# Optimization experiments

Hardware: AMD Instinct MI355X
Metric: run time of the kernel (lower is better)

The kernel has to match this reference:

```python
import jax, jax.numpy as jnp
import numpy as np

B, S, E, H = 2, 2048, 1024, 16
D = E // H  # head_dim = 64


def setup_inputs() -> dict:
    key = jax.random.key(0)
    ks = jax.random.split(key, 5)
    return {
        "hidden_states": jax.random.normal(ks[0], (B, S, E), jnp.float32),
        "c_attn_w": jax.random.normal(ks[1], (E, 3 * E), jnp.float32) * 0.02,
        "c_attn_b": jnp.zeros((3 * E,), jnp.float32),
        "c_proj_w": jax.random.normal(ks[2], (E, E), jnp.float32) * 0.02,
        "c_proj_b": jnp.zeros((E,), jnp.float32),
    }


def reference(hidden_states, c_attn_w, c_attn_b, c_proj_w, c_proj_b):
    # Conv1D: x @ w + b -> qkv [B, S, 3E]
    qkv = hidden_states @ c_attn_w + c_attn_b
    q, k, v = jnp.split(qkv, 3, axis=-1)
    # [B, H, S, D]
    q = q.reshape(B, S, H, D).transpose(0, 2, 1, 3)
    k = k.reshape(B, S, H, D).transpose(0, 2, 1, 3)
    v = v.reshape(B, S, H, D).transpose(0, 2, 1, 3)
    # scores [B, H, S, S], scaled by sqrt(head_dim)
    scores = jnp.einsum("bhqd,bhkd->bhqk", q, k) / jnp.sqrt(jnp.asarray(D, q.dtype))
    causal = jnp.tril(jnp.ones((S, S), bool))  # [S, S]
    mask_value = jnp.finfo(scores.dtype).min
    scores = jnp.where(causal, scores, mask_value)
    attn = jax.nn.softmax(scores, axis=-1)
    # attn @ V -> [B, H, S, D] -> [B, S, E]
    out = jnp.einsum("bhqk,bhkd->bhqd", attn, v)
    out = out.transpose(0, 2, 1, 3).reshape(B, S, E)
    return out @ c_proj_w + c_proj_b
```

## Files before the change

### kernel.cpp

```cpp
#include <hip/hip_runtime.h>

using bf16 = __bf16;
typedef __bf16 bf16x8 __attribute__((ext_vector_type(8)));
typedef __bf16 bf16x4 __attribute__((ext_vector_type(4)));
typedef float  f32x4  __attribute__((ext_vector_type(4)));

#define MFMA16(a, b, c) __builtin_amdgcn_mfma_f32_16x16x32_bf16((a), (b), (c), 0, 0, 0)

static constexpr int S = 2048, E = 1024;
static constexpr float CSCALE = 0.18033688011112042f;

__device__ __forceinline__ void gld16(const bf16* g, bf16* l) {
    __builtin_amdgcn_global_load_lds((const __attribute__((address_space(1))) unsigned*)g,
                                     (__attribute__((address_space(3))) unsigned*)l, 16, 0, 0);
}

__global__ __launch_bounds__(256) void k_prep(const float* __restrict__ hs, const float* __restrict__ w0,
                                              const float* __restrict__ w1, bf16* __restrict__ A0,
                                              bf16* __restrict__ Wt0, bf16* __restrict__ Wt1) {
    __shared__ float tile[32][33];
    const int bx = blockIdx.x;
    if (bx < 4096) {
        int i = (bx * 256 + threadIdx.x) * 4;
        float4 v = *(const float4*)(hs + i);
        bf16x4 o = { (bf16)v.x, (bf16)v.y, (bf16)v.z, (bf16)v.w };
        *(bf16x4*)(A0 + i) = o;
        return;
    }
    const float* in;
    bf16* outp;
    int K, N, nb, kb;
    if (bx < 4096 + 3072) {
        int j = bx - 4096; in = w0; outp = Wt0; K = 1024; N = 3072; nb = j % 96; kb = j / 96;
    } else {
        int j = bx - 7168; in = w1; outp = Wt1; K = 1024; N = 1024; nb = j % 32; kb = j / 32;
    }
    const int bxx = nb * 32, byy = kb * 32;
    const int tx = threadIdx.x & 31, ty = threadIdx.x >> 5;
#pragma unroll
    for (int i = 0; i < 32; i += 8)
        tile[ty + i][tx] = in[(long)(byy + ty + i) * N + bxx + tx];
    __syncthreads();
#pragma unroll
    for (int i = 0; i < 32; i += 8)
        outp[(long)(bxx + ty + i) * K + byy + tx] = (bf16)tile[tx][ty + i];
}

__global__ __launch_bounds__(384, 3) void k_gemm_qkv(const bf16* __restrict__ A, const bf16* __restrict__ Bt,
                                                     const float* __restrict__ bias, bf16* __restrict__ Qs,
                                                     bf16* __restrict__ Kf, bf16* __restrict__ Vf, int Kk) {
    __shared__ __align__(16) char smem[61440];
    bf16* sA = (bf16*)smem;
    bf16* sB = (bf16*)(smem + 24576);

    const int NT = Kk >> 5;

    const int bid = blockIdx.x;
    const int sid = (bid & 7) * 64 + (bid >> 3);
    const long bm = (long)(sid & 31) * 128;
    const long bn = (long)(sid >> 5) * 192;

    const int tid = threadIdx.x;
    const int w = tid >> 6, lane = tid & 63;
    const int col = lane & 15, quad = lane >> 4;
    const int wc = w % 3, wr = w / 3;
    const int wrow = wr * 64, wcol = wc * 64;

    const int nch = (w < 2) ? 4 : 3;
    const bf16* gsrc[4];
    bf16* ldst[4];
    int sstep[4];
#pragma unroll
    for (int j = 0; j < 4; ++j) {
        const int c = w + 6 * j;
        const bool a = (c < 8);
        const int cl = a ? c : (c - 8);
        const int r = cl * 16 + (lane >> 2);
        const int kc = (lane & 3) ^ ((r >> 1) & 3);
        gsrc[j] = (a ? A + (bm + r) * Kk : Bt + (bn + r) * Kk) + kc * 8;
        ldst[j] = (a ? sA : sB) + r * 32 + (lane & 3) * 8;
        sstep[j] = a ? 4096 : 6144;
    }

    f32x4 acc[4][4] = {};

#pragma unroll
    for (int tt = 0; tt < 2; ++tt)
#pragma unroll
        for (int j = 0; j < 4; ++j)
            if (j < nch) gld16(gsrc[j] + tt * 32, ldst[j] + tt * sstep[j]);
    if (w < 2) asm volatile("s_waitcnt vmcnt(4)" ::: "memory");
    else       asm volatile("s_waitcnt vmcnt(3)" ::: "memory");
    __builtin_amdgcn_s_barrier();

    int slot = 0, wslot = 2;
#pragma unroll 1
    for (int t = 0; t < NT; ++t) {
        const bf16* sAs = sA + slot * 4096;
        const bf16* sBs = sB + slot * 6144;

        if (t + 2 < NT) {
#pragma unroll
            for (int j = 0; j < 4; ++j)
                if (j < nch) gld16(gsrc[j] + (t + 2) * 32, ldst[j] + wslot * sstep[j]);
        }

        bf16x8 af[4], bfr[4];
#pragma unroll
        for (int mt = 0; mt < 4; ++mt) {
            const int row = wrow + mt * 16 + col;
            af[mt] = *(const bf16x8*)(sAs + row * 32 + ((quad ^ ((row >> 1) & 3)) * 8));
        }
#pragma unroll
        for (int nt = 0; nt < 4; ++nt) {
            const int row = wcol + nt * 16 + col;
            bfr[nt] = *(const bf16x8*)(sBs + row * 32 + ((quad ^ ((row >> 1) & 3)) * 8));
        }
        __builtin_amdgcn_s_barrier();
        __builtin_amdgcn_s_setprio(1);
#pragma unroll
        for (int mt = 0; mt < 4; ++mt)
#pragma unroll
            for (int nt = 0; nt < 4; ++nt)
                acc[mt][nt] = MFMA16(af[mt], bfr[nt], acc[mt][nt]);
        __builtin_amdgcn_s_setprio(0);
        if (t < NT - 2) {
            if (w < 2) asm volatile("s_waitcnt vmcnt(4)" ::: "memory");
            else       asm volatile("s_waitcnt vmcnt(3)" ::: "memory");
        } else {
            asm volatile("s_waitcnt vmcnt(0)" ::: "memory");
        }
        __builtin_amdgcn_s_barrier();

        slot = (slot == 2) ? 0 : slot + 1;
        wslot = (wslot == 2) ? 0 : wslot + 1;
    }

    const long gc0 = bn + wcol;
    const int seg = (int)(gc0 >> 10);
    float bv[4];
#pragma unroll
    for (int nt = 0; nt < 4; ++nt) bv[nt] = bias[gc0 + nt * 16 + col];

    if (seg == 0) {
#pragma unroll
        for (int nt = 0; nt < 4; ++nt) {
            const long gc = gc0 + nt * 16 + col;
#pragma unroll
            for (int mt = 0; mt < 4; ++mt) {
                const long gr = bm + wrow + mt * 16 + quad * 4;
#pragma unroll
                for (int r = 0; r < 4; ++r)
                    Qs[(gr + r) * 1024 + gc] = (bf16)((acc[mt][nt][r] + bv[nt]) * CSCALE);
            }
        }
        return;
    }

    bf16* myT = (bf16*)smem + w * 4608;
    const int bmi = (int)bm;
    const int b = bmi >> 11;
    const int ktw = ((bmi & 2047) >> 6) + wr;
    const int head = (int)((gc0 & 1023) >> 6);
    const int bh = b * 16 + head;

    if (seg == 1) {
#pragma unroll
        for (int mt = 0; mt < 4; ++mt)
#pragma unroll
            for (int nt = 0; nt < 4; ++nt)
#pragma unroll
                for (int r = 0; r < 4; ++r)
                    myT[(mt * 16 + quad * 4 + r) * 72 + nt * 16 + col] = (bf16)(acc[mt][nt][r] + bv[nt]);
#pragma unroll
        for (int mtp = 0; mtp < 4; ++mtp)
#pragma unroll
            for (int half = 0; half < 2; ++half) {
                bf16x8 ch = *(const bf16x8*)(myT + (mtp * 16 + col) * 72 + half * 32 + quad * 8);
                const long chunk = ((long)(bh * 32 + ktw) * 8 + mtp * 2 + half) * 64 + lane;
                *(bf16x8*)(Kf + chunk * 8) = ch;
            }
    } else {
#pragma unroll
        for (int nt = 0; nt < 4; ++nt)
#pragma unroll
            for (int mt = 0; mt < 4; ++mt) {
                bf16x4 pk = { (bf16)(acc[mt][nt][0] + bv[nt]), (bf16)(acc[mt][nt][1] + bv[nt]),
                              (bf16)(acc[mt][nt][2] + bv[nt]), (bf16)(acc[mt][nt][3] + bv[nt]) };
                *(bf16x4*)(myT + (nt * 16 + col) * 72 + mt * 16 + quad * 4) = pk;
            }
#pragma unroll
        for (int dt = 0; dt < 4; ++dt)
#pragma unroll
            for (int ks = 0; ks < 2; ++ks) {
                bf16x8 ch = *(const bf16x8*)(myT + (dt * 16 + col) * 72 + ks * 32 + quad * 8);
                const long chunk = ((long)(bh * 32 + ktw) * 8 + dt * 2 + ks) * 64 + lane;
                *(bf16x8*)(Vf + chunk * 8) = ch;
            }
    }
}

__global__ __launch_bounds__(256) void k_gemm_bt64(const bf16* __restrict__ A, const bf16* __restrict__ Bt,
                                                    const float* __restrict__ bias, float* __restrict__ Cout,
                                                    int Mm, int Nn, int Kk) {
    const int bm = blockIdx.x * 64;
    const int bn = blockIdx.y * 128;
    const int tid = threadIdx.x;
    const int w = tid >> 6, lane = tid & 63;
    const int wm = (w >> 1) * 32, wn = (w & 1) * 64;
    const int col = lane & 15, quad = lane >> 4;

    __shared__ bf16 sA[64 * 64];
    __shared__ bf16 sB[128 * 64];

    const bf16* pA[2]; bf16* lA[2];
#pragma unroll
    for (int i = 0; i < 2; i++) {
        const int c = i * 256 + w * 64 + lane;
        const int r = c >> 3, sl = (c & 7) ^ (r & 7);
        pA[i] = A + (long)(bm + r) * Kk + sl * 8;
        lA[i] = sA + i * 2048 + w * 512;
    }
    const bf16* pB[4]; bf16* lB[4];
#pragma unroll
    for (int i = 0; i < 4; i++) {
        const int c = i * 256 + w * 64 + lane;
        const int r = c >> 3, sl = (c & 7) ^ (r & 7);
        pB[i] = Bt + (long)(bn + r) * Kk + sl * 8;
        lB[i] = sB + i * 2048 + w * 512;
    }

    f32x4 acc[2][4] = {};

    for (int k0 = 0; k0 < Kk; k0 += 64) {
        __syncthreads();
#pragma unroll
        for (int i = 0; i < 2; i++) gld16(pA[i] + k0, lA[i]);
#pragma unroll
        for (int i = 0; i < 4; i++) gld16(pB[i] + k0, lB[i]);
        __syncthreads();
#pragma unroll
        for (int h = 0; h < 2; h++) {
            bf16x8 af[2], bfr[4];
#pragma unroll
            for (int mt = 0; mt < 2; mt++) {
                const int row = wm + mt * 16 + col;
                af[mt] = *(const bf16x8*)(sA + row * 64 + (((h * 4 + quad) ^ (col & 7)) * 8));
            }
#pragma unroll
            for (int nt = 0; nt < 4; nt++) {
                const int row = wn + nt * 16 + col;
                bfr[nt] = *(const bf16x8*)(sB + row * 64 + (((h * 4 + quad) ^ (col & 7)) * 8));
            }
#pragma unroll
            for (int mt = 0; mt < 2; mt++)
#pragma unroll
                for (int nt = 0; nt < 4; nt++)
                    acc[mt][nt] = MFMA16(af[mt], bfr[nt], acc[mt][nt]);
        }
    }

#pragma unroll
    for (int mt = 0; mt < 2; mt++) {
        const int gr = bm + wm + mt * 16 + quad * 4;
#pragma unroll
        for (int nt = 0; nt < 4; nt++) {
            const int gc = bn + wn + nt * 16 + col;
            const float bv = bias[gc];
#pragma unroll
            for (int r = 0; r < 4; r++)
                Cout[(long)(gr + r) * Nn + gc] = acc[mt][nt][r] + bv;
        }
    }
}

__global__ __launch_bounds__(128) void k_attn(const bf16* __restrict__ Qs, const bf16* __restrict__ Kf,
                                              const bf16* __restrict__ Vf, bf16* __restrict__ out) {
    const int bh = blockIdx.x & 31;
    const int tp = blockIdx.x >> 5;
    const int b = bh >> 4, h = bh & 15;
    const int tid = threadIdx.x;
    const int w = tid >> 6, lane = tid & 63;
    const int col = lane & 15, quad = lane >> 4;

    __shared__ bf16 sP[2][32 * 72];
    __shared__ float M[2][64][36];
    bf16* pw = sP[w];

    const bf16* kfb = Kf + ((long)bh << 17) + lane * 8;
    const bf16* vfb = Vf + ((long)bh << 17) + lane * 8;

#pragma unroll 1
    for (int sel = 0; sel < 2; sel++) {
        const int t = sel ? 63 - tp : tp;
        const int q0 = t * 32;
        const int nkt = (t >> 1) + 1;
        const int kA = nkt >> 1;
        const int kbeg = w ? kA : 0;
        const int kend = w ? nkt : kA;

        bf16x8 bq[2][2];
#pragma unroll
        for (int qg = 0; qg < 2; qg++) {
            const bf16* qp = Qs + (long)(b * S + q0 + qg * 16 + col) * E + h * 64 + quad * 8;
            bq[qg][0] = *(const bf16x8*)(qp);
            bq[qg][1] = *(const bf16x8*)(qp + 32);
        }
        float m_[2] = { -1e30f, -1e30f }, l_[2] = { 0.f, 0.f };
        f32x4 o[2][4] = {};

#pragma unroll 1
        for (int kt = kbeg; kt < kend; kt++) {
            bf16x8 kfr[4][2], vfr[4][2];
#pragma unroll
            for (int mt = 0; mt < 4; mt++)
#pragma unroll
                for (int half = 0; half < 2; half++)
                    kfr[mt][half] = *(const bf16x8*)(kfb + ((long)(kt * 8 + mt * 2 + half) << 9));
#pragma unroll
            for (int dt = 0; dt < 4; dt++)
#pragma unroll
                for (int ks = 0; ks < 2; ks++)
                    vfr[dt][ks] = *(const bf16x8*)(vfb + ((long)(kt * 8 + dt * 2 + ks) << 9));

            f32x4 s[2][4];
#pragma unroll
            for (int mt = 0; mt < 4; mt++)
#pragma unroll
                for (int qg = 0; qg < 2; qg++) {
                    f32x4 z = {};
                    z = MFMA16(kfr[mt][0], bq[qg][0], z);
                    z = MFMA16(kfr[mt][1], bq[qg][1], z);
                    s[qg][mt] = z;
                }
            if (kt == nkt - 1) {
#pragma unroll
                for (int qg = 0; qg < 2; qg++) {
                    const int qrow = q0 + qg * 16 + col;
#pragma unroll
                    for (int mt = 0; mt < 4; mt++)
#pragma unroll
                        for (int r = 0; r < 4; r++)
                            if (kt * 64 + mt * 16 + quad * 4 + r > qrow) s[qg][mt][r] = -1e30f;
                }
            }
#pragma unroll
            for (int qg = 0; qg < 2; qg++) {
                float cm = -1e30f;
#pragma unroll
                for (int mt = 0; mt < 4; mt++)
#pragma unroll
                    for (int r = 0; r < 4; r++) cm = fmaxf(cm, s[qg][mt][r]);
                cm = fmaxf(cm, __shfl_xor(cm, 16));
                cm = fmaxf(cm, __shfl_xor(cm, 32));
                const float mnew = fmaxf(m_[qg], cm);
                const float alpha = __builtin_amdgcn_exp2f(m_[qg] - mnew);
                m_[qg] = mnew;
                float rs = 0.f;
#pragma unroll
                for (int mt = 0; mt < 4; mt++)
#pragma unroll
                    for (int r = 0; r < 4; r++) {
                        float pe = __builtin_amdgcn_exp2f(s[qg][mt][r] - mnew);
                        s[qg][mt][r] = pe;
                        rs += pe;
                    }
                l_[qg] = l_[qg] * alpha + rs;
#pragma unroll
                for (int dt = 0; dt < 4; dt++)
#pragma unroll
                    for (int r = 0; r < 4; r++) o[qg][dt][r] *= alpha;
#pragma unroll
                for (int mt = 0; mt < 4; mt++) {
                    bf16x4 pk = { (bf16)s[qg][mt][0], (bf16)s[qg][mt][1],
                                  (bf16)s[qg][mt][2], (bf16)s[qg][mt][3] };
                    *(bf16x4*)(pw + (qg * 16 + col) * 72 + mt * 16 + quad * 4) = pk;
                }
            }
#pragma unroll
            for (int ks = 0; ks < 2; ks++) {
                bf16x8 ap[2];
#pragma unroll
                for (int qg = 0; qg < 2; qg++)
                    ap[qg] = *(const bf16x8*)(pw + (qg * 16 + col) * 72 + ks * 32 + quad * 8);
#pragma unroll
                for (int dt = 0; dt < 4; dt++)
#pragma unroll
                    for (int qg = 0; qg < 2; qg++)
                        o[qg][dt] = MFMA16(vfr[dt][ks], ap[qg], o[qg][dt]);
            }
        }

#pragma unroll
        for (int qg = 0; qg < 2; qg++) {
            float lt = l_[qg];
            lt += __shfl_xor(lt, 16);
            lt += __shfl_xor(lt, 32);
            l_[qg] = lt;
        }

        if (w == 0) {
#pragma unroll
            for (int qg = 0; qg < 2; qg++) {
#pragma unroll
                for (int dt = 0; dt < 4; dt++)
                    *(f32x4*)&M[sel][lane][qg * 16 + dt * 4] = o[qg][dt];
                M[sel][lane][32 + qg * 2] = m_[qg];
                M[sel][lane][33 + qg * 2] = l_[qg];
            }
        }
        __syncthreads();
        if (w == 1) {
#pragma unroll
            for (int qg = 0; qg < 2; qg++) {
                const float m0 = M[sel][lane][32 + qg * 2];
                const float l0 = M[sel][lane][33 + qg * 2];
                const float mm = fmaxf(m0, m_[qg]);
                const float a0 = __builtin_amdgcn_exp2f(m0 - mm);
                const float a1 = __builtin_amdgcn_exp2f(m_[qg] - mm);
                const float li = 1.f / (l0 * a0 + l_[qg] * a1);
                bf16* op = out + (long)(b * S + q0 + qg * 16 + col) * E + h * 64 + quad * 4;
#pragma unroll
                for (int dt = 0; dt < 4; dt++) {
                    f32x4 o0 = *(const f32x4*)&M[sel][lane][qg * 16 + dt * 4];
                    bf16x4 ov;
#pragma unroll
                    for (int r = 0; r < 4; r++)
                        ov[r] = (bf16)((o0[r] * a0 + o[qg][dt][r] * a1) * li);
                    *(bf16x4*)(op + dt * 16) = ov;
                }
            }
        }
    }
}

extern "C" void kernel_launch(void* const* d_in, const int* in_sizes, int n_in,
                              void* d_out, int out_size, void* d_ws, size_t ws_size,
                              hipStream_t stream) {
    const float* hs = (const float*)d_in[0];
    const float* w0 = (const float*)d_in[1];
    const float* b0 = (const float*)d_in[2];
    const float* w1 = (const float*)d_in[3];
    const float* b1 = (const float*)d_in[4];
    float* outp = (float*)d_out;

    char* ws = (char*)d_ws;
    bf16* A0    = (bf16*)(ws);
    bf16* Wt0   = (bf16*)(ws + 8388608);
    bf16* Wt1   = (bf16*)(ws + 14680064);
    bf16* Qs    = (bf16*)(ws + 16777216);
    bf16* Kf    = (bf16*)(ws + 25165824);
    bf16* Vf    = (bf16*)(ws + 33554432);
    bf16* attnO = (bf16*)(ws + 41943040);

    k_prep<<<8192, 256, 0, stream>>>(hs, w0, w1, A0, Wt0, Wt1);
    k_gemm_qkv<<<512, 384, 0, stream>>>(A0, Wt0, b0, Qs, Kf, Vf, 1024);
    k_attn<<<1024, 128, 0, stream>>>(Qs, Kf, Vf, attnO);
    k_gemm_bt64<<<dim3(64, 8), 256, 0, stream>>>(attnO, Wt1, b1, outp, 4096, 1024, 1024);
}
```

Baseline: 179.0 us.

## Pre-swizzle QKV weights into MFMA fragment layout and load B directly to registers

The prep kernel now writes the QKV weight transpose in an MFMA-fragment-ordered layout. The QKV GEMM then loads each wave's B operand straight from global memory into registers with dwordx4 loads, double-buffered across two register sets, instead of staging it through LDS. LDS usage drops to the A tiles only, and the epilogue transposes in two halves to fit the smaller buffer. This removes LDS traffic and bandwidth for B and may raise occupancy. The cost is more VGPR pressure, and each wave reads its weights from global memory with no sharing across the waves that use the same columns.

```diff
diff --git a/kernel.cpp b/kernel.cpp
--- a/kernel.cpp
+++ b/kernel.cpp
@@ -13,6 +13,15 @@
 __device__ __forceinline__ void gld16(const bf16* g, bf16* l) {
     __builtin_amdgcn_global_load_lds((const __attribute__((address_space(1))) unsigned*)g,
                                      (__attribute__((address_space(3))) unsigned*)l, 16, 0, 0);
+}
+
+__device__ __forceinline__ void gload4(const bf16* p, bf16x8& r0, bf16x8& r1, bf16x8& r2, bf16x8& r3) {
+    asm volatile("global_load_dwordx4 %0, %4, off\n\t"
+                 "global_load_dwordx4 %1, %4, off offset:1024\n\t"
+                 "global_load_dwordx4 %2, %4, off offset:2048\n\t"
+                 "global_load_dwordx4 %3, %4, off offset:3072"
+                 : "=&v"(r0), "=&v"(r1), "=&v"(r2), "=&v"(r3)
+                 : "v"(p));
 }
 
 __global__ __launch_bounds__(256) void k_prep(const float* __restrict__ hs, const float* __restrict__ w0,
@@ -30,10 +39,11 @@
     const float* in;
     bf16* outp;
     int K, N, nb, kb;
+    bool frag;
     if (bx < 4096 + 3072) {
-        int j = bx - 4096; in = w0; outp = Wt0; K = 1024; N = 3072; nb = j % 96; kb = j / 96;
+        int j = bx - 4096; in = w0; outp = Wt0; K = 1024; N = 3072; nb = j % 96; kb = j / 96; frag = true;
     } else {
-        int j = bx - 7168; in = w1; outp = Wt1; K = 1024; N = 1024; nb = j % 32; kb = j / 32;
+        int j = bx - 7168; in = w1; outp = Wt1; K = 1024; N = 1024; nb = j % 32; kb = j / 32; frag = false;
     }
     const int bxx = nb * 32, byy = kb * 32;
     const int tx = threadIdx.x & 31, ty = threadIdx.x >> 5;
@@ -41,17 +51,30 @@
     for (int i = 0; i < 32; i += 8)
         tile[ty + i][tx] = in[(long)(byy + ty + i) * N + bxx + tx];
     __syncthreads();
-#pragma unroll
-    for (int i = 0; i < 32; i += 8)
-        outp[(long)(bxx + ty + i) * K + byy + tx] = (bf16)tile[tx][ty + i];
+    if (frag) {
+        if (threadIdx.x < 128) {
+            const int nl = threadIdx.x >> 2;
+            const int kq = threadIdx.x & 3;
+            const int n = bxx + nl, k = byy + kq * 8;
+            bf16x8 v;
+#pragma unroll
+            for (int e = 0; e < 8; ++e) v[e] = (bf16)tile[kq * 8 + e][nl];
+            const long addr = (((long)(n >> 6) * 32 + (k >> 5)) * 4 + ((n >> 4) & 3)) * 512
+                            + ((k >> 3) & 3) * 128 + (n & 15) * 8;
+            *(bf16x8*)(outp + addr) = v;
+        }
+    } else {
+#pragma unroll
+        for (int i = 0; i < 32; i += 8)
+            outp[(long)(bxx + ty + i) * K + byy + tx] = (bf16)tile[tx][ty + i];
+    }
 }
 
 __global__ __launch_bounds__(384, 3) void k_gemm_qkv(const bf16* __restrict__ A, const bf16* __restrict__ Bt,
                                                      const float* __restrict__ bias, bf16* __restrict__ Qs,
                                                      bf16* __restrict__ Kf, bf16* __restrict__ Vf, int Kk) {
-    __shared__ __align__(16) char smem[61440];
+    __shared__ __align__(16) char smem[28672];
     bf16* sA = (bf16*)smem;
-    bf16* sB = (bf16*)(smem + 24576);
 
     const int NT = Kk >> 5;
 
@@ -66,75 +89,70 @@
     const int wc = w % 3, wr = w / 3;
     const int wrow = wr * 64, wcol = wc * 64;
 
-    const int nch = (w < 2) ? 4 : 3;
-    const bf16* gsrc[4];
-    bf16* ldst[4];
-    int sstep[4];
-#pragma unroll
-    for (int j = 0; j < 4; ++j) {
-        const int c = w + 6 * j;
-        const bool a = (c < 8);
-        const int cl = a ? c : (c - 8);
-        const int r = cl * 16 + (lane >> 2);
-        const int kc = (lane & 3) ^ ((r >> 1) & 3);
-        gsrc[j] = (a ? A + (bm + r) * Kk : Bt + (bn + r) * Kk) + kc * 8;
-        ldst[j] = (a ? sA : sB) + r * 32 + (lane & 3) * 8;
-        sstep[j] = a ? 4096 : 6144;
-    }
+    const int u0 = w * 64 + lane;
+    const int r0s = u0 >> 2, kq0 = u0 & 3;
+    const bf16* gA0 = A + (bm + r0s) * Kk + ((kq0 ^ ((r0s >> 1) & 3)) * 8);
+    const int u1 = 384 + ((w & 1) * 64) + lane;
+    const int r1s = u1 >> 2, kq1 = u1 & 3;
+    const bf16* gA1 = A + (bm + r1s) * Kk + ((kq1 ^ ((r1s >> 1) & 3)) * 8);
+
+    const int strip = (int)(sid >> 5) * 3 + wc;
+    const bf16* wfb = Bt + (long)strip * 65536 + lane * 8;
 
     f32x4 acc[4][4] = {};
-
-#pragma unroll
-    for (int tt = 0; tt < 2; ++tt)
-#pragma unroll
-        for (int j = 0; j < 4; ++j)
-            if (j < nch) gld16(gsrc[j] + tt * 32, ldst[j] + tt * sstep[j]);
-    if (w < 2) asm volatile("s_waitcnt vmcnt(4)" ::: "memory");
-    else       asm volatile("s_waitcnt vmcnt(3)" ::: "memory");
+    bf16x8 b00, b01, b02, b03, b10, b11, b12, b13;
+
+    gld16(gA0, sA + u0 * 8);
+    if (w < 2) gld16(gA1, sA + u1 * 8);
+    gld16(gA0 + 32, sA + 4096 + u0 * 8);
+    if (w < 2) gld16(gA1 + 32, sA + 4096 + u1 * 8);
+    gload4(wfb, b00, b01, b02, b03);
+    gload4(wfb + 2048, b10, b11, b12, b13);
+    asm volatile("s_waitcnt vmcnt(4)" ::: "memory");
     __builtin_amdgcn_s_barrier();
-
-    int slot = 0, wslot = 2;
+    __builtin_amdgcn_sched_barrier(0);
+
+#define QSTEP(T, B0, B1, B2, B3) do {                                                     \
+    const int t_ = (T);                                                                   \
+    const bf16* sAs = sA + (t_ % 3) * 4096;                                               \
+    bf16x8 af0, af1, af2, af3;                                                            \
+    { const int r_ = wrow + col;      af0 = *(const bf16x8*)(sAs + r_ * 32 + ((quad ^ ((r_ >> 1) & 3)) * 8)); } \
+    { const int r_ = wrow + 16 + col; af1 = *(const bf16x8*)(sAs + r_ * 32 + ((quad ^ ((r_ >> 1) & 3)) * 8)); } \
+    { const int r_ = wrow + 32 + col; af2 = *(const bf16x8*)(sAs + r_ * 32 + ((quad ^ ((r_ >> 1) & 3)) * 8)); } \
+    { const int r_ = wrow + 48 + col; af3 = *(const bf16x8*)(sAs + r_ * 32 + ((quad ^ ((r_ >> 1) & 3)) * 8)); } \
+    const bool pf_ = (t_ + 2 < NT);                                                       \
+    if (pf_) {             \
+        bf16* dA = sA + ((t_ + 2) % 3) * 4096;                                            \
+        gld16(gA0 + (t_ + 2) * 32, dA + u0 * 8);                                          \
+        if (w < 2) gld16(gA1 + (t_ + 2) * 32, dA + u1 * 8);                               \
+    }                                                                                     \
+    __builtin_amdgcn_s_setprio(1);                                                        \
+    acc[0][0] = MFMA16(af0, B0, acc[0][0]); acc[0][1] = MFMA16(af0, B1, acc[0][1]);       \
+    acc[0][2] = MFMA16(af0, B2, acc[0][2]); acc[0][3] = MFMA16(af0, B3, acc[0][3]);       \
+    acc[1][0] = MFMA16(af1, B0, acc[1][0]); acc[1][1] = MFMA16(af1, B1, acc[1][1]);       \
+    acc[1][2] = MFMA16(af1, B2, acc[1][2]); acc[1][3] = MFMA16(af1, B3, acc[1][3]);       \
+    acc[2][0] = MFMA16(af2, B0, acc[2][0]); acc[2][1] = MFMA16(af2, B1, acc[2][1]);       \
+    acc[2][2] = MFMA16(af2, B2, acc[2][2]); acc[2][3] = MFMA16(af2, B3, acc[2][3]);       \
+    acc[3][0] = MFMA16(af3, B0, acc[3][0]); acc[3][1] = MFMA16(af3, B1, acc[3][1]);       \
+    acc[3][2] = MFMA16(af3, B2, acc[3][2]); acc[3][3] = MFMA16(af3, B3, acc[3][3]);       \
+    __builtin_amdgcn_s_setprio(0);                                                        \
+    if (pf_) gload4(wfb + (long)(t_ + 2) * 2048, B0, B1, B2, B3);   \
+    if (t_ < NT - 2) {                                                                    \
+        if (w < 2) asm volatile("s_waitcnt vmcnt(6)" ::: "memory");                       \
+        else       asm volatile("s_waitcnt vmcnt(5)" ::: "memory");                       \
+    } else {                                                                              \
+        asm volatile("s_waitcnt vmcnt(0)" ::: "memory");                                  \
+    }                                                                                     \
+    __builtin_amdgcn_s_barrier();                                                         \
+    __builtin_amdgcn_sched_barrier(0);                                                    \
+} while (0)
+
 #pragma unroll 1
-    for (int t = 0; t < NT; ++t) {
-        const bf16* sAs = sA + slot * 4096;
-        const bf16* sBs = sB + slot * 6144;
-
-        if (t + 2 < NT) {
-#pragma unroll
-            for (int j = 0; j < 4; ++j)
-                if (j < nch) gld16(gsrc[j] + (t + 2) * 32, ldst[j] + wslot * sstep[j]);
-        }
-
-        bf16x8 af[4], bfr[4];
-#pragma unroll
-        for (int mt = 0; mt < 4; ++mt) {
-            const int row = wrow + mt * 16 + col;
-            af[mt] = *(const bf16x8*)(sAs + row * 32 + ((quad ^ ((row >> 1) & 3)) * 8));
-        }
-#pragma unroll
-        for (int nt = 0; nt < 4; ++nt) {
-            const int row = wcol + nt * 16 + col;
-            bfr[nt] = *(const bf16x8*)(sBs + row * 32 + ((quad ^ ((row >> 1) & 3)) * 8));
-        }
-        __builtin_amdgcn_s_barrier();
-        __builtin_amdgcn_s_setprio(1);
-#pragma unroll
-        for (int mt = 0; mt < 4; ++mt)
-#pragma unroll
-            for (int nt = 0; nt < 4; ++nt)
-                acc[mt][nt] = MFMA16(af[mt], bfr[nt], acc[mt][nt]);
-        __builtin_amdgcn_s_setprio(0);
-        if (t < NT - 2) {
-            if (w < 2) asm volatile("s_waitcnt vmcnt(4)" ::: "memory");
-            else       asm volatile("s_waitcnt vmcnt(3)" ::: "memory");
-        } else {
-            asm volatile("s_waitcnt vmcnt(0)" ::: "memory");
-        }
-        __builtin_amdgcn_s_barrier();
-
-        slot = (slot == 2) ? 0 : slot + 1;
-        wslot = (wslot == 2) ? 0 : wslot + 1;
-    }
+    for (int t = 0; t < NT; t += 2) {
+        QSTEP(t,     b00, b01, b02, b03);
+        QSTEP(t + 1, b10, b11, b12, b13);
+    }
+#undef QSTEP
 
     const long gc0 = bn + wcol;
     const int seg = (int)(gc0 >> 10);
@@ -157,7 +175,7 @@
         return;
     }
 
-    bf16* myT = (bf16*)smem + w * 4608;
+    bf16* myT = (bf16*)smem + w * 2304;
     const int bmi = (int)bm;
     const int b = bmi >> 11;
     const int ktw = ((bmi & 2047) >> 6) + wr;
@@ -166,37 +184,48 @@
 
     if (seg == 1) {
 #pragma unroll
-        for (int mt = 0; mt < 4; ++mt)
-#pragma unroll
-            for (int nt = 0; nt < 4; ++nt)
-#pragma unroll
-                for (int r = 0; r < 4; ++r)
-                    myT[(mt * 16 + quad * 4 + r) * 72 + nt * 16 + col] = (bf16)(acc[mt][nt][r] + bv[nt]);
-#pragma unroll
-        for (int mtp = 0; mtp < 4; ++mtp)
-#pragma unroll
-            for (int half = 0; half < 2; ++half) {
-                bf16x8 ch = *(const bf16x8*)(myT + (mtp * 16 + col) * 72 + half * 32 + quad * 8);
-                const long chunk = ((long)(bh * 32 + ktw) * 8 + mtp * 2 + half) * 64 + lane;
+        for (int h = 0; h < 2; ++h) {
+#pragma unroll
+            for (int mt = 0; mt < 4; ++mt)
+#pragma unroll
+                for (int nt2 = 0; nt2 < 2; ++nt2) {
+                    const int nt = 2 * h + nt2;
+#pragma unroll
+                    for (int r = 0; r < 4; ++r)
+                        myT[(mt * 16 + quad * 4 + r) * 36 + nt2 * 16 + col] =
+                            (bf16)(acc[mt][nt][r] + bv[nt]);
+                }
+#pragma unroll
+            for (int mtp = 0; mtp < 4; ++mtp) {
+                bf16x8 ch = *(const bf16x8*)(myT + (mtp * 16 + col) * 36 + quad * 8);
+                const long chunk = ((long)(bh * 32 + ktw) * 8 + mtp * 2 + h) * 64 + lane;
                 *(bf16x8*)(Kf + chunk * 8) = ch;
             }
+        }
     } else {
 #pragma unroll
-        for (int nt = 0; nt < 4; ++nt)
-#pragma unroll
-            for (int mt = 0; mt < 4; ++mt) {
-                bf16x4 pk = { (bf16)(acc[mt][nt][0] + bv[nt]), (bf16)(acc[mt][nt][1] + bv[nt]),
-                              (bf16)(acc[mt][nt][2] + bv[nt]), (bf16)(acc[mt][nt][3] + bv[nt]) };
-                *(bf16x4*)(myT + (nt * 16 + col) * 72 + mt * 16 + quad * 4) = pk;
-            }
-#pragma unroll
-        for (int dt = 0; dt < 4; ++dt)
-#pragma unroll
-            for (int ks = 0; ks < 2; ++ks) {
-                bf16x8 ch = *(const bf16x8*)(myT + (dt * 16 + col) * 72 + ks * 32 + quad * 8);
-                const long chunk = ((long)(bh * 32 + ktw) * 8 + dt * 2 + ks) * 64 + lane;
-                *(bf16x8*)(Vf + chunk * 8) = ch;
-            }
+        for (int h = 0; h < 2; ++h) {
+#pragma unroll
+            for (int nt2 = 0; nt2 < 2; ++nt2) {
+                const int nt = 2 * h + nt2;
+#pragma unroll
+                for (int mt = 0; mt < 4; ++mt) {
+                    bf16x4 pk = { (bf16)(acc[mt][nt][0] + bv[nt]), (bf16)(acc[mt][nt][1] + bv[nt]),
+                                  (bf16)(acc[mt][nt][2] + bv[nt]), (bf16)(acc[mt][nt][3] + bv[nt]) };
+                    *(bf16x4*)(myT + (nt2 * 16 + col) * 72 + mt * 16 + quad * 4) = pk;
+                }
+            }
+#pragma unroll
+            for (int dt2 = 0; dt2 < 2; ++dt2) {
+                const int dt = 2 * h + dt2;
+#pragma unroll
+                for (int ks = 0; ks < 2; ++ks) {
+                    bf16x8 ch = *(const bf16x8*)(myT + (dt2 * 16 + col) * 72 + ks * 32 + quad * 8);
+                    const long chunk = ((long)(bh * 32 + ktw) * 8 + dt * 2 + ks) * 64 + lane;
+                    *(bf16x8*)(Vf + chunk * 8) = ch;
+                }
+            }
+        }
     }
 }
 
```

After: 175.2 us. -2.1%, faster.
